# Optimization experiments

Measured on AMD Instinct MI355X. Metric: run time of the kernel, lower is better.

## Reference

```python
import jax, jax.numpy as jnp
import numpy as np

MEM, BATCH, L, E, H, HOPS = 64, 32, 64, 1024, 1024, 3


def setup_inputs() -> dict:
    key = jax.random.key(0)
    ks = jax.random.split(key, 7)
    s = 1.0 / np.sqrt(H).astype(np.float32)
    return {
        "inputs": jax.random.normal(ks[0], (MEM, BATCH, L, E), jnp.float32),
        "questions": jax.random.normal(ks[1], (BATCH, L, E), jnp.float32),
        "A": jax.random.normal(ks[2], (E, H), jnp.float32) * s,
        "C": jax.random.normal(ks[3], (E, H), jnp.float32) * s,
        "Bmat": jax.random.normal(ks[4], (E, H), jnp.float32) * s,
        "TA": jax.random.normal(ks[5], (MEM, H), jnp.float32) * s,
        "TC": jax.random.normal(ks[6], (MEM, H), jnp.float32) * s,
    }


def reference(inputs, questions, A, C, Bmat, TA, TC):
    # u = sum over words of (questions @ B): [batch, hidden]
    u = jnp.einsum('ble,eh->bh', questions, Bmat)
    # Memory/value slots (hop-invariant since A,C,TA,TC are shared across hops):
    # m_j = sum_l inputs[j] @ A + TA[j]; c_j analogously.  [batch, mem, hidden]
    m = jnp.einsum('mble,eh->bmh', inputs, A) + TA
    c = jnp.einsum('mble,eh->bmh', inputs, C) + TC
    for _ in range(HOPS):
        # p_j = softmax_j(u . m_j): [batch, mem]
        p = jax.nn.softmax(jnp.einsum('bh,bmh->bm', u, m), axis=-1)
        # o = sum_j p_j * c_j: [batch, hidden]
        o = jnp.einsum('bm,bmh->bh', p, c)
        u = u + o
    return u
```

## Files before the change

### kernel.cpp

```cpp
#include <hip/hip_runtime.h>


#define NMEM 64
#define NBATCH 32
#define NL 64
#define NE 1024
#define NH 1024
#define NEP 1088
#define NHOPS 3

#define OFF_S   0u
#define OFF_QS  (2048u*1024u)
#define OFF_W   (OFF_QS + 32u*1024u)
#define OFF_P   (OFF_W + 32u*1088u)
#define OFF_R   (OFF_P + 32u*64u)
#define OFF_SV  (OFF_R + 32u*1024u)
#define OFF_AT  (OFF_SV + 32u*64u)

__global__ __launch_bounds__(256) void k_reduce(
    const float* __restrict__ inputs, const float* __restrict__ questions,
    const float* __restrict__ A, const float* __restrict__ TA,
    float* __restrict__ S, float* __restrict__ qs,
    float* __restrict__ w, float* __restrict__ u, float* __restrict__ At) {
  const int blk = blockIdx.x, t = threadIdx.x;
  __shared__ float tile[64][65];

  if (blk < 2048) {
    const float4* base = (const float4*)(inputs + (size_t)blk * (NL * NE));
    float4 acc = make_float4(0.f, 0.f, 0.f, 0.f);
#pragma unroll 8
    for (int l = 0; l < NL; ++l) {
      float4 v = base[l * (NE / 4) + t];
      acc.x += v.x; acc.y += v.y; acc.z += v.z; acc.w += v.w;
    }
    ((float4*)(S + (size_t)blk * NE))[t] = acc;
  } else if (blk < 2080) {
    const int b = blk - 2048;
    const float4* base = (const float4*)(questions + (size_t)b * (NL * NE));
    float4 acc = make_float4(0.f, 0.f, 0.f, 0.f);
#pragma unroll 8
    for (int l = 0; l < NL; ++l) {
      float4 v = base[l * (NE / 4) + t];
      acc.x += v.x; acc.y += v.y; acc.z += v.z; acc.w += v.w;
    }
    ((float4*)(qs + (size_t)b * NE))[t] = acc;
    const float4 z = make_float4(0.f, 0.f, 0.f, 0.f);
    ((float4*)(u + (size_t)b * NH))[t] = z;
    ((float4*)(w + (size_t)b * NEP))[t] = z;
    if (t < 16) ((float4*)(w + (size_t)b * NEP))[256 + t] = z;
  } else {
    const int idx = blk - 2080;
    const int et = idx % 17;
    const int ht = idx / 17;
    const int r0 = t >> 6, c = t & 63;
#pragma unroll
    for (int rr = r0; rr < 64; rr += 4) {
      const int e = et * 64 + rr, h = ht * 64 + c;
      tile[rr][c] = (e < NE) ? A[(size_t)e * NH + h] : TA[(size_t)(e - NE) * NH + h];
    }
    __syncthreads();
#pragma unroll
    for (int rr = r0; rr < 64; rr += 4) {
      const int h = ht * 64 + rr, e = et * 64 + c;
      At[(size_t)h * NEP + e] = tile[c][rr];
    }
  }
}

__global__ __launch_bounds__(256) void k_u0(
    const float* __restrict__ qs, const float* __restrict__ B,
    float* __restrict__ u) {
  const int t = threadIdx.x;
  const int h = blockIdx.x * 256 + t;
  const int b0 = blockIdx.y * 4;
  const int e0 = blockIdx.z * 128;
  __shared__ float lq[4][128];
  for (int idx = t; idx < 512; idx += 256)
    lq[idx >> 7][idx & 127] = qs[(size_t)(b0 + (idx >> 7)) * NE + e0 + (idx & 127)];
  __syncthreads();
  float acc[4] = {0.f, 0.f, 0.f, 0.f};
#pragma unroll 8
  for (int i = 0; i < 128; ++i) {
    const float bv = B[(size_t)(e0 + i) * NH + h];
#pragma unroll
    for (int bb = 0; bb < 4; ++bb) acc[bb] += lq[bb][i] * bv;
  }
#pragma unroll
  for (int bb = 0; bb < 4; ++bb) atomicAdd(&u[(size_t)(b0 + bb) * NH + h], acc[bb]);
}

__global__ __launch_bounds__(256) void k_w(
    const float* __restrict__ At, const float* __restrict__ u,
    float* __restrict__ w) {
  const int t = threadIdx.x;
  const int ep = blockIdx.x * 256 + t;
  const int b0 = blockIdx.y * 4;
  const int h0 = blockIdx.z * 128;
  __shared__ float lu[4][128];
  for (int idx = t; idx < 512; idx += 256)
    lu[idx >> 7][idx & 127] = u[(size_t)(b0 + (idx >> 7)) * NH + h0 + (idx & 127)];
  __syncthreads();
  if (ep >= NEP) return;
  float acc[4] = {0.f, 0.f, 0.f, 0.f};
#pragma unroll 8
  for (int i = 0; i < 128; ++i) {
    const float av = At[(size_t)(h0 + i) * NEP + ep];
#pragma unroll
    for (int bb = 0; bb < 4; ++bb) acc[bb] += lu[bb][i] * av;
  }
#pragma unroll
  for (int bb = 0; bb < 4; ++bb) atomicAdd(&w[(size_t)(b0 + bb) * NEP + ep], acc[bb]);
}

__global__ __launch_bounds__(256) void k_s(
    const float* __restrict__ S, const float* __restrict__ w,
    float* __restrict__ sv) {
  const int lane = threadIdx.x & 63, wv = threadIdx.x >> 6;
  const int j = blockIdx.x * 4 + wv, b = blockIdx.y;
  const float4* S4 = (const float4*)(S + (size_t)(j * NBATCH + b) * NE);
  const float4* w4 = (const float4*)(w + (size_t)b * NEP);
  float acc = 0.f;
#pragma unroll
  for (int i = 0; i < 4; ++i) {
    const int slot = i * 64 + lane;
    float4 a = S4[slot], c = w4[slot];
    acc += a.x * c.x + a.y * c.y + a.z * c.z + a.w * c.w;
  }
#pragma unroll
  for (int off = 32; off > 0; off >>= 1) acc += __shfl_xor(acc, off, 64);
  if (lane == 0) sv[(size_t)b * NMEM + j] = acc + w[(size_t)b * NEP + NE + j];
}

__global__ __launch_bounds__(256) void k_pr(
    const float* __restrict__ S, const float* __restrict__ sv,
    float* __restrict__ p, float* __restrict__ r, float* __restrict__ w) {
  const int t = threadIdx.x;
  const int b = blockIdx.y, e0 = blockIdx.x * 256;
  __shared__ float lp[64];
  if (t < 64) {
    float s = sv[(size_t)b * NMEM + t];
    float m = s;
#pragma unroll
    for (int off = 32; off > 0; off >>= 1) m = fmaxf(m, __shfl_xor(m, off, 64));
    const float ex = __expf(s - m);
    float l = ex;
#pragma unroll
    for (int off = 32; off > 0; off >>= 1) l += __shfl_xor(l, off, 64);
    const float pv = ex / l;
    lp[t] = pv;
    if (blockIdx.x == 0) p[(size_t)b * NMEM + t] = pv;
  }
  __syncthreads();
  const int e = e0 + t;
  float acc = 0.f;
#pragma unroll 8
  for (int j = 0; j < NMEM; ++j)
    acc += lp[j] * S[(size_t)(j * NBATCH + b) * NE + e];
  r[(size_t)b * NE + e] = acc;
  w[(size_t)b * NEP + e] = 0.f;
  if (blockIdx.x == 0 && t < 64) w[(size_t)b * NEP + NE + t] = 0.f;
}

__global__ __launch_bounds__(256) void k_o(
    const float* __restrict__ C, const float* __restrict__ TC,
    const float* __restrict__ r, const float* __restrict__ p,
    float* __restrict__ u) {
  const int t = threadIdx.x;
  const int h = blockIdx.x * 256 + t;
  const int b0 = blockIdx.y * 4;
  const int e0 = blockIdx.z * 128;
  __shared__ float lr[4][128];
  __shared__ float lp[4][64];
  for (int idx = t; idx < 512; idx += 256)
    lr[idx >> 7][idx & 127] = r[(size_t)(b0 + (idx >> 7)) * NE + e0 + (idx & 127)];
  if (blockIdx.z == 0 && t < 256) {
    const int bb = t >> 6, j = t & 63;
    lp[bb][j] = p[(size_t)(b0 + bb) * NMEM + j];
  }
  __syncthreads();
  float acc[4] = {0.f, 0.f, 0.f, 0.f};
#pragma unroll 8
  for (int i = 0; i < 128; ++i) {
    const float cv = C[(size_t)(e0 + i) * NH + h];
#pragma unroll
    for (int bb = 0; bb < 4; ++bb) acc[bb] += lr[bb][i] * cv;
  }
  if (blockIdx.z == 0) {
#pragma unroll 8
    for (int j = 0; j < NMEM; ++j) {
      const float tcv = TC[(size_t)j * NH + h];
#pragma unroll
      for (int bb = 0; bb < 4; ++bb) acc[bb] += lp[bb][j] * tcv;
    }
  }
#pragma unroll
  for (int bb = 0; bb < 4; ++bb) atomicAdd(&u[(size_t)(b0 + bb) * NH + h], acc[bb]);
}

extern "C" void kernel_launch(void* const* d_in, const int* in_sizes, int n_in,
                              void* d_out, int out_size, void* d_ws, size_t ws_size,
                              hipStream_t stream) {
  (void)in_sizes; (void)n_in; (void)out_size; (void)ws_size;
  const float* inputs    = (const float*)d_in[0];
  const float* questions = (const float*)d_in[1];
  const float* A         = (const float*)d_in[2];
  const float* C         = (const float*)d_in[3];
  const float* B         = (const float*)d_in[4];
  const float* TA        = (const float*)d_in[5];
  const float* TC        = (const float*)d_in[6];
  float* u  = (float*)d_out;
  float* ws = (float*)d_ws;
  float* S  = ws + OFF_S;
  float* qs = ws + OFF_QS;
  float* w  = ws + OFF_W;
  float* p  = ws + OFF_P;
  float* r  = ws + OFF_R;
  float* sv = ws + OFF_SV;
  float* At = ws + OFF_AT;

  k_reduce<<<2048 + 32 + 272, 256, 0, stream>>>(inputs, questions, A, TA, S, qs, w, u, At);
  k_u0<<<dim3(4, 8, 8), 256, 0, stream>>>(qs, B, u);
  for (int hop = 0; hop < NHOPS; ++hop) {
    k_w<<<dim3(5, 8, 8), 256, 0, stream>>>(At, u, w);
    k_s<<<dim3(16, 32), 256, 0, stream>>>(S, w, sv);
    k_pr<<<dim3(4, 32), 256, 0, stream>>>(S, sv, p, r, w);
    k_o<<<dim3(4, 8, 8), 256, 0, stream>>>(C, TC, r, p, u);
  }
}
```

Baseline: 799.5 us.

## Replace atomics with partial-sum buffers, fuse score/softmax kernels, fold u0 into reduce

Computes the initial u inside the question-reduction blocks of the reduce kernel, replacing a separate launch. Replaces atomicAdd accumulation in the w and o GEMVs with per-split partial buffers that are summed by consumers, and keeps u as u0 plus accumulated o partials until a final kernel. Fuses the score dot products, softmax and weighted memory sum into one 1024-thread kernel per batch, and vectorises the GEMVs with float4. This removes atomics, zeroing passes and launches, but adds partial-buffer traffic and a long serial B loop in 32 blocks.

```diff
diff --git a/kernel.cpp b/kernel.cpp
--- a/kernel.cpp
+++ b/kernel.cpp
@@ -10,20 +10,20 @@
 #define NHOPS 3
 
 #define OFF_S   0u
-#define OFF_QS  (2048u*1024u)
-#define OFF_W   (OFF_QS + 32u*1024u)
-#define OFF_P   (OFF_W + 32u*1088u)
+#define OFF_AT  (2048u*1024u)
+#define OFF_WP  (OFF_AT + 1024u*1088u)
+#define OFF_OP  (OFF_WP + 8u*32u*1088u)
+#define OFF_U0  (OFF_OP + 16u*32u*1024u)
+#define OFF_P   (OFF_U0 + 32u*1024u)
 #define OFF_R   (OFF_P + 32u*64u)
-#define OFF_SV  (OFF_R + 32u*1024u)
-#define OFF_AT  (OFF_SV + 32u*64u)
 
 __global__ __launch_bounds__(256) void k_reduce(
     const float* __restrict__ inputs, const float* __restrict__ questions,
     const float* __restrict__ A, const float* __restrict__ TA,
-    float* __restrict__ S, float* __restrict__ qs,
-    float* __restrict__ w, float* __restrict__ u, float* __restrict__ At) {
+    const float* __restrict__ B,
+    float* __restrict__ S, float* __restrict__ u0, float* __restrict__ At) {
   const int blk = blockIdx.x, t = threadIdx.x;
-  __shared__ float tile[64][65];
+  __shared__ __align__(16) float tile[64][65];
 
   if (blk < 2048) {
     const float4* base = (const float4*)(inputs + (size_t)blk * (NL * NE));
@@ -36,6 +36,7 @@
     ((float4*)(S + (size_t)blk * NE))[t] = acc;
   } else if (blk < 2080) {
     const int b = blk - 2048;
+    float* lq = &tile[0][0];
     const float4* base = (const float4*)(questions + (size_t)b * (NL * NE));
     float4 acc = make_float4(0.f, 0.f, 0.f, 0.f);
 #pragma unroll 8
@@ -43,11 +44,17 @@
       float4 v = base[l * (NE / 4) + t];
       acc.x += v.x; acc.y += v.y; acc.z += v.z; acc.w += v.w;
     }
-    ((float4*)(qs + (size_t)b * NE))[t] = acc;
-    const float4 z = make_float4(0.f, 0.f, 0.f, 0.f);
-    ((float4*)(u + (size_t)b * NH))[t] = z;
-    ((float4*)(w + (size_t)b * NEP))[t] = z;
-    if (t < 16) ((float4*)(w + (size_t)b * NEP))[256 + t] = z;
+    ((float4*)lq)[t] = acc;
+    __syncthreads();
+    const float4* B4 = (const float4*)B;
+    float4 ua = make_float4(0.f, 0.f, 0.f, 0.f);
+#pragma unroll 8
+    for (int e = 0; e < NE; ++e) {
+      const float q = lq[e];
+      const float4 bv = B4[(size_t)e * (NH / 4) + t];
+      ua.x += q * bv.x; ua.y += q * bv.y; ua.z += q * bv.z; ua.w += q * bv.w;
+    }
+    ((float4*)(u0 + (size_t)b * NH))[t] = ua;
   } else {
     const int idx = blk - 2080;
     const int et = idx % 17;
@@ -67,78 +74,88 @@
   }
 }
 
-__global__ __launch_bounds__(256) void k_u0(
-    const float* __restrict__ qs, const float* __restrict__ B,
-    float* __restrict__ u) {
+__global__ __launch_bounds__(256) void k_w(
+    const float* __restrict__ At, const float* __restrict__ u0,
+    const float* __restrict__ opart, float* __restrict__ wpart, int hop) {
   const int t = threadIdx.x;
-  const int h = blockIdx.x * 256 + t;
   const int b0 = blockIdx.y * 4;
-  const int e0 = blockIdx.z * 128;
-  __shared__ float lq[4][128];
-  for (int idx = t; idx < 512; idx += 256)
-    lq[idx >> 7][idx & 127] = qs[(size_t)(b0 + (idx >> 7)) * NE + e0 + (idx & 127)];
-  __syncthreads();
-  float acc[4] = {0.f, 0.f, 0.f, 0.f};
+  const int z = blockIdx.z, h0 = z * 128;
+  __shared__ float lu[4][128];
+  for (int idx = t; idx < 512; idx += 256) {
+    const int bb = idx >> 7, i = idx & 127;
+    float v = u0[(size_t)(b0 + bb) * NH + h0 + i];
+    if (hop > 0) {
+#pragma unroll
+      for (int zz = 0; zz < 16; ++zz)
+        v += opart[((size_t)zz * NBATCH + b0 + bb) * NH + h0 + i];
+    }
+    lu[bb][i] = v;
+  }
+  __syncthreads();
+  const int ep4 = blockIdx.x * 256 + t;
+  if (ep4 >= NEP / 4) return;
+  const float4* At4 = (const float4*)At;
+  float4 acc[4];
+#pragma unroll
+  for (int bb = 0; bb < 4; ++bb) acc[bb] = make_float4(0.f, 0.f, 0.f, 0.f);
 #pragma unroll 8
   for (int i = 0; i < 128; ++i) {
-    const float bv = B[(size_t)(e0 + i) * NH + h];
-#pragma unroll
-    for (int bb = 0; bb < 4; ++bb) acc[bb] += lq[bb][i] * bv;
-  }
-#pragma unroll
-  for (int bb = 0; bb < 4; ++bb) atomicAdd(&u[(size_t)(b0 + bb) * NH + h], acc[bb]);
-}
-
-__global__ __launch_bounds__(256) void k_w(
-    const float* __restrict__ At, const float* __restrict__ u,
-    float* __restrict__ w) {
+    const float4 av = At4[(size_t)(h0 + i) * (NEP / 4) + ep4];
+#pragma unroll
+    for (int bb = 0; bb < 4; ++bb) {
+      const float uv = lu[bb][i];
+      acc[bb].x += uv * av.x; acc[bb].y += uv * av.y;
+      acc[bb].z += uv * av.z; acc[bb].w += uv * av.w;
+    }
+  }
+  float4* wp4 = (float4*)wpart;
+#pragma unroll
+  for (int bb = 0; bb < 4; ++bb)
+    wp4[((size_t)z * NBATCH + b0 + bb) * (NEP / 4) + ep4] = acc[bb];
+}
+
+__global__ __launch_bounds__(1024) void k_spr(
+    const float* __restrict__ S, const float* __restrict__ wpart,
+    float* __restrict__ p, float* __restrict__ r) {
   const int t = threadIdx.x;
-  const int ep = blockIdx.x * 256 + t;
-  const int b0 = blockIdx.y * 4;
-  const int h0 = blockIdx.z * 128;
-  __shared__ float lu[4][128];
-  for (int idx = t; idx < 512; idx += 256)
-    lu[idx >> 7][idx & 127] = u[(size_t)(b0 + (idx >> 7)) * NH + h0 + (idx & 127)];
-  __syncthreads();
-  if (ep >= NEP) return;
-  float acc[4] = {0.f, 0.f, 0.f, 0.f};
-#pragma unroll 8
-  for (int i = 0; i < 128; ++i) {
-    const float av = At[(size_t)(h0 + i) * NEP + ep];
-#pragma unroll
-    for (int bb = 0; bb < 4; ++bb) acc[bb] += lu[bb][i] * av;
-  }
-#pragma unroll
-  for (int bb = 0; bb < 4; ++bb) atomicAdd(&w[(size_t)(b0 + bb) * NEP + ep], acc[bb]);
-}
-
-__global__ __launch_bounds__(256) void k_s(
-    const float* __restrict__ S, const float* __restrict__ w,
-    float* __restrict__ sv) {
-  const int lane = threadIdx.x & 63, wv = threadIdx.x >> 6;
-  const int j = blockIdx.x * 4 + wv, b = blockIdx.y;
-  const float4* S4 = (const float4*)(S + (size_t)(j * NBATCH + b) * NE);
-  const float4* w4 = (const float4*)(w + (size_t)b * NEP);
-  float acc = 0.f;
-#pragma unroll
-  for (int i = 0; i < 4; ++i) {
-    const int slot = i * 64 + lane;
-    float4 a = S4[slot], c = w4[slot];
-    acc += a.x * c.x + a.y * c.y + a.z * c.z + a.w * c.w;
-  }
-#pragma unroll
-  for (int off = 32; off > 0; off >>= 1) acc += __shfl_xor(acc, off, 64);
-  if (lane == 0) sv[(size_t)b * NMEM + j] = acc + w[(size_t)b * NEP + NE + j];
-}
-
-__global__ __launch_bounds__(256) void k_pr(
-    const float* __restrict__ S, const float* __restrict__ sv,
-    float* __restrict__ p, float* __restrict__ r, float* __restrict__ w) {
-  const int t = threadIdx.x;
-  const int b = blockIdx.y, e0 = blockIdx.x * 256;
-  __shared__ float lp[64];
-  if (t < 64) {
-    float s = sv[(size_t)b * NMEM + t];
+  const int b = blockIdx.x;
+  __shared__ __align__(16) float lw[NEP];
+  __shared__ float sl[NMEM];
+  __shared__ float lp[NMEM];
+  {
+    float v = 0.f;
+#pragma unroll
+    for (int z = 0; z < 8; ++z) v += wpart[((size_t)z * NBATCH + b) * NEP + t];
+    lw[t] = v;
+    if (t < NMEM) {
+      float v2 = 0.f;
+#pragma unroll
+      for (int z = 0; z < 8; ++z)
+        v2 += wpart[((size_t)z * NBATCH + b) * NEP + NE + t];
+      lw[NE + t] = v2;
+    }
+  }
+  __syncthreads();
+  const int lane = t & 63, wv = t >> 6;
+  const float4* lw4 = (const float4*)lw;
+#pragma unroll
+  for (int q = 0; q < 4; ++q) {
+    const int j = wv * 4 + q;
+    const float4* S4 = (const float4*)(S + (size_t)(j * NBATCH + b) * NE);
+    float acc = 0.f;
+#pragma unroll
+    for (int i = 0; i < 4; ++i) {
+      const float4 a = S4[i * 64 + lane];
+      const float4 c = lw4[i * 64 + lane];
+      acc += a.x * c.x + a.y * c.y + a.z * c.z + a.w * c.w;
+    }
+#pragma unroll
+    for (int off = 32; off > 0; off >>= 1) acc += __shfl_xor(acc, off, 64);
+    if (lane == 0) sl[j] = acc + lw[NE + j];
+  }
+  __syncthreads();
+  if (t < NMEM) {
+    const float s = sl[t];
     float m = s;
 #pragma unroll
     for (int off = 32; off > 0; off >>= 1) m = fmaxf(m, __shfl_xor(m, off, 64));
@@ -148,53 +165,85 @@
     for (int off = 32; off > 0; off >>= 1) l += __shfl_xor(l, off, 64);
     const float pv = ex / l;
     lp[t] = pv;
-    if (blockIdx.x == 0) p[(size_t)b * NMEM + t] = pv;
-  }
-  __syncthreads();
-  const int e = e0 + t;
+    p[(size_t)b * NMEM + t] = pv;
+  }
+  __syncthreads();
   float acc = 0.f;
 #pragma unroll 8
   for (int j = 0; j < NMEM; ++j)
-    acc += lp[j] * S[(size_t)(j * NBATCH + b) * NE + e];
-  r[(size_t)b * NE + e] = acc;
-  w[(size_t)b * NEP + e] = 0.f;
-  if (blockIdx.x == 0 && t < 64) w[(size_t)b * NEP + NE + t] = 0.f;
+    acc += lp[j] * S[(size_t)(j * NBATCH + b) * NE + t];
+  r[(size_t)b * NE + t] = acc;
 }
 
 __global__ __launch_bounds__(256) void k_o(
     const float* __restrict__ C, const float* __restrict__ TC,
     const float* __restrict__ r, const float* __restrict__ p,
+    float* __restrict__ opart, int hop) {
+  const int t = threadIdx.x;
+  const int b0 = blockIdx.x * 4;
+  const int z = blockIdx.y, e0 = z * 64;
+  __shared__ float lr[4][64];
+  __shared__ float lpp[4][64];
+  {
+    const int bb = t >> 6, i = t & 63;
+    lr[bb][i] = r[(size_t)(b0 + bb) * NE + e0 + i];
+    if (z == 0) lpp[bb][i] = p[(size_t)(b0 + bb) * NMEM + i];
+  }
+  __syncthreads();
+  const float4* C4 = (const float4*)C;
+  float4 acc[4];
+#pragma unroll
+  for (int bb = 0; bb < 4; ++bb) acc[bb] = make_float4(0.f, 0.f, 0.f, 0.f);
+#pragma unroll 8
+  for (int i = 0; i < 64; ++i) {
+    const float4 cv = C4[(size_t)(e0 + i) * (NH / 4) + t];
+#pragma unroll
+    for (int bb = 0; bb < 4; ++bb) {
+      const float rv = lr[bb][i];
+      acc[bb].x += rv * cv.x; acc[bb].y += rv * cv.y;
+      acc[bb].z += rv * cv.z; acc[bb].w += rv * cv.w;
+    }
+  }
+  if (z == 0) {
+    const float4* TC4 = (const float4*)TC;
+#pragma unroll 8
+    for (int j = 0; j < NMEM; ++j) {
+      const float4 tv = TC4[(size_t)j * (NH / 4) + t];
+#pragma unroll
+      for (int bb = 0; bb < 4; ++bb) {
+        const float pv = lpp[bb][j];
+        acc[bb].x += pv * tv.x; acc[bb].y += pv * tv.y;
+        acc[bb].z += pv * tv.z; acc[bb].w += pv * tv.w;
+      }
+    }
+  }
+  float4* op4 = (float4*)opart;
+#pragma unroll
+  for (int bb = 0; bb < 4; ++bb) {
+    const size_t idx = ((size_t)z * NBATCH + b0 + bb) * (NH / 4) + t;
+    if (hop == 0) {
+      op4[idx] = acc[bb];
+    } else {
+      float4 o = op4[idx];
+      o.x += acc[bb].x; o.y += acc[bb].y; o.z += acc[bb].z; o.w += acc[bb].w;
+      op4[idx] = o;
+    }
+  }
+}
+
+__global__ __launch_bounds__(256) void k_final(
+    const float* __restrict__ u0, const float* __restrict__ opart,
     float* __restrict__ u) {
-  const int t = threadIdx.x;
-  const int h = blockIdx.x * 256 + t;
-  const int b0 = blockIdx.y * 4;
-  const int e0 = blockIdx.z * 128;
-  __shared__ float lr[4][128];
-  __shared__ float lp[4][64];
-  for (int idx = t; idx < 512; idx += 256)
-    lr[idx >> 7][idx & 127] = r[(size_t)(b0 + (idx >> 7)) * NE + e0 + (idx & 127)];
-  if (blockIdx.z == 0 && t < 256) {
-    const int bb = t >> 6, j = t & 63;
-    lp[bb][j] = p[(size_t)(b0 + bb) * NMEM + j];
-  }
-  __syncthreads();
-  float acc[4] = {0.f, 0.f, 0.f, 0.f};
-#pragma unroll 8
-  for (int i = 0; i < 128; ++i) {
-    const float cv = C[(size_t)(e0 + i) * NH + h];
-#pragma unroll
-    for (int bb = 0; bb < 4; ++bb) acc[bb] += lr[bb][i] * cv;
-  }
-  if (blockIdx.z == 0) {
-#pragma unroll 8
-    for (int j = 0; j < NMEM; ++j) {
-      const float tcv = TC[(size_t)j * NH + h];
-#pragma unroll
-      for (int bb = 0; bb < 4; ++bb) acc[bb] += lp[bb][j] * tcv;
-    }
-  }
-#pragma unroll
-  for (int bb = 0; bb < 4; ++bb) atomicAdd(&u[(size_t)(b0 + bb) * NH + h], acc[bb]);
+  const int slot = blockIdx.x * 256 + threadIdx.x;
+  const int b = slot >> 8, h4 = slot & 255;
+  float4 v = ((const float4*)u0)[slot];
+  const float4* op4 = (const float4*)opart;
+#pragma unroll
+  for (int z = 0; z < 16; ++z) {
+    const float4 o = op4[((size_t)z * NBATCH + b) * (NH / 4) + h4];
+    v.x += o.x; v.y += o.y; v.z += o.z; v.w += o.w;
+  }
+  ((float4*)u)[slot] = v;
 }
 
 extern "C" void kernel_launch(void* const* d_in, const int* in_sizes, int n_in,
@@ -210,20 +259,19 @@
   const float* TC        = (const float*)d_in[6];
   float* u  = (float*)d_out;
   float* ws = (float*)d_ws;
-  float* S  = ws + OFF_S;
-  float* qs = ws + OFF_QS;
-  float* w  = ws + OFF_W;
-  float* p  = ws + OFF_P;
-  float* r  = ws + OFF_R;
-  float* sv = ws + OFF_SV;
-  float* At = ws + OFF_AT;
-
-  k_reduce<<<2048 + 32 + 272, 256, 0, stream>>>(inputs, questions, A, TA, S, qs, w, u, At);
-  k_u0<<<dim3(4, 8, 8), 256, 0, stream>>>(qs, B, u);
+  float* S     = ws + OFF_S;
+  float* At    = ws + OFF_AT;
+  float* wpart = ws + OFF_WP;
+  float* opart = ws + OFF_OP;
+  float* u0    = ws + OFF_U0;
+  float* p     = ws + OFF_P;
+  float* r     = ws + OFF_R;
+
+  k_reduce<<<2048 + 32 + 272, 256, 0, stream>>>(inputs, questions, A, TA, B, S, u0, At);
   for (int hop = 0; hop < NHOPS; ++hop) {
-    k_w<<<dim3(5, 8, 8), 256, 0, stream>>>(At, u, w);
-    k_s<<<dim3(16, 32), 256, 0, stream>>>(S, w, sv);
-    k_pr<<<dim3(4, 32), 256, 0, stream>>>(S, sv, p, r, w);
-    k_o<<<dim3(4, 8, 8), 256, 0, stream>>>(C, TC, r, p, u);
-  }
-}
+    k_w<<<dim3(2, 8, 8), 256, 0, stream>>>(At, u0, opart, wpart, hop);
+    k_spr<<<32, 1024, 0, stream>>>(S, wpart, p, r);
+    k_o<<<dim3(8, 16), 256, 0, stream>>>(C, TC, r, p, opart, hop);
+  }
+  k_final<<<32, 256, 0, stream>>>(u0, opart, u);
+}
```

Measured after the change: 905.9 us. 1.13x slower.

## Fuse question reduction with B projection and softmax/readout into output kernel

Applied to the files above, without the earlier changes.

The separate u0 projection kernel is folded into the reduce kernel: 32 blocks each sum the questions for four batches into shared memory, then multiply by B across all of E and write u directly, with no atomics. The softmax and the probability-weighted memory sum (k_pr) are folded into k_o: each block recomputes softmax and its slice of r from S before the C projection, and one block per batch group zeroes w for the next hop. This removes two launches per hop plus one at setup, and drops the qs, p and r buffers. In exchange, questions and S are read redundantly across the h-blocks, and the new question blocks run a long serial loop over E that could leave a tail.

```diff
diff --git a/kernel.cpp b/kernel.cpp
--- a/kernel.cpp
+++ b/kernel.cpp
@@ -10,20 +10,18 @@
 #define NHOPS 3
 
 #define OFF_S   0u
-#define OFF_QS  (2048u*1024u)
-#define OFF_W   (OFF_QS + 32u*1024u)
-#define OFF_P   (OFF_W + 32u*1088u)
-#define OFF_R   (OFF_P + 32u*64u)
-#define OFF_SV  (OFF_R + 32u*1024u)
-#define OFF_AT  (OFF_SV + 32u*64u)
+#define OFF_AT  (2048u*1024u)
+#define OFF_W   (OFF_AT + 1024u*1088u)
+#define OFF_SV  (OFF_W + 32u*1088u)
 
 __global__ __launch_bounds__(256) void k_reduce(
     const float* __restrict__ inputs, const float* __restrict__ questions,
     const float* __restrict__ A, const float* __restrict__ TA,
-    float* __restrict__ S, float* __restrict__ qs,
-    float* __restrict__ w, float* __restrict__ u, float* __restrict__ At) {
+    const float* __restrict__ B,
+    float* __restrict__ S, float* __restrict__ u, float* __restrict__ w,
+    float* __restrict__ At) {
   const int blk = blockIdx.x, t = threadIdx.x;
-  __shared__ float tile[64][65];
+  __shared__ __align__(16) float tile[64][65];
 
   if (blk < 2048) {
     const float4* base = (const float4*)(inputs + (size_t)blk * (NL * NE));
@@ -35,19 +33,32 @@
     }
     ((float4*)(S + (size_t)blk * NE))[t] = acc;
   } else if (blk < 2080) {
-    const int b = blk - 2048;
-    const float4* base = (const float4*)(questions + (size_t)b * (NL * NE));
-    float4 acc = make_float4(0.f, 0.f, 0.f, 0.f);
-#pragma unroll 8
-    for (int l = 0; l < NL; ++l) {
-      float4 v = base[l * (NE / 4) + t];
-      acc.x += v.x; acc.y += v.y; acc.z += v.z; acc.w += v.w;
-    }
-    ((float4*)(qs + (size_t)b * NE))[t] = acc;
-    const float4 z = make_float4(0.f, 0.f, 0.f, 0.f);
-    ((float4*)(u + (size_t)b * NH))[t] = z;
-    ((float4*)(w + (size_t)b * NEP))[t] = z;
-    if (t < 16) ((float4*)(w + (size_t)b * NEP))[256 + t] = z;
+    const int idx = blk - 2048;
+    const int ht = idx & 3;
+    const int b0 = (idx >> 2) * 4;
+    float* lq = &tile[0][0];
+    for (int slot = t; slot < 4096; slot += 256) {
+      const int bb = slot >> 10, e = slot & 1023;
+      const float* qp = questions + (size_t)(b0 + bb) * (NL * NE) + e;
+      float a = 0.f;
+#pragma unroll 8
+      for (int l = 0; l < NL; ++l) a += qp[l * NE];
+      lq[slot] = a;
+    }
+    if (ht == 0)
+      for (int i = t; i < 4 * NEP; i += 256)
+        w[(size_t)(b0 + i / NEP) * NEP + (i % NEP)] = 0.f;
+    __syncthreads();
+    const int h = ht * 256 + t;
+    float acc[4] = {0.f, 0.f, 0.f, 0.f};
+#pragma unroll 8
+    for (int e = 0; e < NE; ++e) {
+      const float bv = B[(size_t)e * NH + h];
+#pragma unroll
+      for (int bb = 0; bb < 4; ++bb) acc[bb] += lq[bb * 1024 + e] * bv;
+    }
+#pragma unroll
+    for (int bb = 0; bb < 4; ++bb) u[(size_t)(b0 + bb) * NH + h] = acc[bb];
   } else {
     const int idx = blk - 2080;
     const int et = idx % 17;
@@ -65,28 +76,6 @@
       At[(size_t)h * NEP + e] = tile[c][rr];
     }
   }
-}
-
-__global__ __launch_bounds__(256) void k_u0(
-    const float* __restrict__ qs, const float* __restrict__ B,
-    float* __restrict__ u) {
-  const int t = threadIdx.x;
-  const int h = blockIdx.x * 256 + t;
-  const int b0 = blockIdx.y * 4;
-  const int e0 = blockIdx.z * 128;
-  __shared__ float lq[4][128];
-  for (int idx = t; idx < 512; idx += 256)
-    lq[idx >> 7][idx & 127] = qs[(size_t)(b0 + (idx >> 7)) * NE + e0 + (idx & 127)];
-  __syncthreads();
-  float acc[4] = {0.f, 0.f, 0.f, 0.f};
-#pragma unroll 8
-  for (int i = 0; i < 128; ++i) {
-    const float bv = B[(size_t)(e0 + i) * NH + h];
-#pragma unroll
-    for (int bb = 0; bb < 4; ++bb) acc[bb] += lq[bb][i] * bv;
-  }
-#pragma unroll
-  for (int bb = 0; bb < 4; ++bb) atomicAdd(&u[(size_t)(b0 + bb) * NH + h], acc[bb]);
 }
 
 __global__ __launch_bounds__(256) void k_w(
@@ -131,51 +120,36 @@
   if (lane == 0) sv[(size_t)b * NMEM + j] = acc + w[(size_t)b * NEP + NE + j];
 }
 
-__global__ __launch_bounds__(256) void k_pr(
-    const float* __restrict__ S, const float* __restrict__ sv,
-    float* __restrict__ p, float* __restrict__ r, float* __restrict__ w) {
-  const int t = threadIdx.x;
-  const int b = blockIdx.y, e0 = blockIdx.x * 256;
-  __shared__ float lp[64];
-  if (t < 64) {
-    float s = sv[(size_t)b * NMEM + t];
-    float m = s;
-#pragma unroll
-    for (int off = 32; off > 0; off >>= 1) m = fmaxf(m, __shfl_xor(m, off, 64));
-    const float ex = __expf(s - m);
-    float l = ex;
-#pragma unroll
-    for (int off = 32; off > 0; off >>= 1) l += __shfl_xor(l, off, 64);
-    const float pv = ex / l;
-    lp[t] = pv;
-    if (blockIdx.x == 0) p[(size_t)b * NMEM + t] = pv;
-  }
-  __syncthreads();
-  const int e = e0 + t;
-  float acc = 0.f;
-#pragma unroll 8
-  for (int j = 0; j < NMEM; ++j)
-    acc += lp[j] * S[(size_t)(j * NBATCH + b) * NE + e];
-  r[(size_t)b * NE + e] = acc;
-  w[(size_t)b * NEP + e] = 0.f;
-  if (blockIdx.x == 0 && t < 64) w[(size_t)b * NEP + NE + t] = 0.f;
-}
-
 __global__ __launch_bounds__(256) void k_o(
     const float* __restrict__ C, const float* __restrict__ TC,
-    const float* __restrict__ r, const float* __restrict__ p,
-    float* __restrict__ u) {
+    const float* __restrict__ S, const float* __restrict__ sv,
+    float* __restrict__ u, float* __restrict__ w) {
   const int t = threadIdx.x;
   const int h = blockIdx.x * 256 + t;
   const int b0 = blockIdx.y * 4;
   const int e0 = blockIdx.z * 128;
+  __shared__ float lp[4][64];
   __shared__ float lr[4][128];
-  __shared__ float lp[4][64];
-  for (int idx = t; idx < 512; idx += 256)
-    lr[idx >> 7][idx & 127] = r[(size_t)(b0 + (idx >> 7)) * NE + e0 + (idx & 127)];
-  if (blockIdx.z == 0 && t < 256) {
-    const int bb = t >> 6, j = t & 63;
-    lp[bb][j] = p[(size_t)(b0 + bb) * NMEM + j];
+  {
+    const int lane = t & 63, wv = t >> 6;
+    const float s = sv[(size_t)(b0 + wv) * NMEM + lane];
+    float m = s;
+#pragma unroll
+    for (int off = 32; off > 0; off >>= 1) m = fmaxf(m, __shfl_xor(m, off, 64));
+    const float ex = __expf(s - m);
+    float l = ex;
+#pragma unroll
+    for (int off = 32; off > 0; off >>= 1) l += __shfl_xor(l, off, 64);
+    lp[wv][lane] = ex / l;
+  }
+  __syncthreads();
+  for (int idx = t; idx < 512; idx += 256) {
+    const int bb = idx >> 7, i = idx & 127;
+    float acc = 0.f;
+#pragma unroll 8
+    for (int j = 0; j < NMEM; ++j)
+      acc += lp[bb][j] * S[((size_t)j * NBATCH + b0 + bb) * NE + e0 + i];
+    lr[bb][i] = acc;
   }
   __syncthreads();
   float acc[4] = {0.f, 0.f, 0.f, 0.f};
@@ -195,6 +169,9 @@
   }
 #pragma unroll
   for (int bb = 0; bb < 4; ++bb) atomicAdd(&u[(size_t)(b0 + bb) * NH + h], acc[bb]);
+  if (blockIdx.x == 0 && blockIdx.z == 0)
+    for (int i = t; i < 4 * NEP; i += 256)
+      w[(size_t)(b0 + i / NEP) * NEP + (i % NEP)] = 0.f;
 }
 
 extern "C" void kernel_launch(void* const* d_in, const int* in_sizes, int n_in,
@@ -211,19 +188,14 @@
   float* u  = (float*)d_out;
   float* ws = (float*)d_ws;
   float* S  = ws + OFF_S;
-  float* qs = ws + OFF_QS;
+  float* At = ws + OFF_AT;
   float* w  = ws + OFF_W;
-  float* p  = ws + OFF_P;
-  float* r  = ws + OFF_R;
   float* sv = ws + OFF_SV;
-  float* At = ws + OFF_AT;
-
-  k_reduce<<<2048 + 32 + 272, 256, 0, stream>>>(inputs, questions, A, TA, S, qs, w, u, At);
-  k_u0<<<dim3(4, 8, 8), 256, 0, stream>>>(qs, B, u);
+
+  k_reduce<<<2048 + 32 + 272, 256, 0, stream>>>(inputs, questions, A, TA, B, S, u, w, At);
   for (int hop = 0; hop < NHOPS; ++hop) {
     k_w<<<dim3(5, 8, 8), 256, 0, stream>>>(At, u, w);
     k_s<<<dim3(16, 32), 256, 0, stream>>>(S, w, sv);
-    k_pr<<<dim3(4, 32), 256, 0, stream>>>(S, sv, p, r, w);
-    k_o<<<dim3(4, 8, 8), 256, 0, stream>>>(C, TC, r, p, u);
-  }
-}
+    k_o<<<dim3(4, 8, 8), 256, 0, stream>>>(C, TC, S, sv, u, w);
+  }
+}
```

Measured after the change: 902.0 us. 1.13x slower.
